# Kernel tuning notes

Measured on AMD Instinct MI355X. Metric: run time of the kernel, lower is better.

## Reference

```python
import jax, jax.numpy as jnp
import numpy as np

H = 64  # hidden size

def lstm_layer(x, h0, c0, Wih, Whh, bih, bhh):
    # x: [B,T,D]; Wih: [4H,D]; Whh: [4H,H]; gate order i,f,g,o (PyTorch)
    xp = jnp.einsum('btd,gd->btg', x, Wih) + bih  # precompute input projections [B,T,4H]
    def step(carry, xt):
        h, c = carry
        gates = xt + h @ Whh.T + bhh
        i, f, g, o = jnp.split(gates, 4, axis=-1)
        c = jax.nn.sigmoid(f) * c + jax.nn.sigmoid(i) * jnp.tanh(g)
        h = jax.nn.sigmoid(o) * jnp.tanh(c)
        return (h, c), h
    (_, _), ys = jax.lax.scan(step, (h0, c0), jnp.swapaxes(xp, 0, 1))  # scan over T
    return jnp.swapaxes(ys, 0, 1)  # [B,T,H]

def setup_inputs() -> dict:
    key = jax.random.key(0)
    ks = jax.random.split(key, 12)
    B, T = 256, 2048
    s = 0.1
    return {
        'input': jax.random.normal(ks[0], (B, T), jnp.float32),
        'h0': jnp.zeros((2, B, H), jnp.float32),
        'c0': jnp.zeros((2, B, H), jnp.float32),
        'Wih0': jax.random.normal(ks[1], (4 * H, 1), jnp.float32) * s,
        'Whh0': jax.random.normal(ks[2], (4 * H, H), jnp.float32) * s,
        'bih0': jax.random.normal(ks[3], (4 * H,), jnp.float32) * s,
        'bhh0': jax.random.normal(ks[4], (4 * H,), jnp.float32) * s,
        'Wih1': jax.random.normal(ks[5], (4 * H, H), jnp.float32) * s,
        'Whh1': jax.random.normal(ks[6], (4 * H, H), jnp.float32) * s,
        'bih1': jax.random.normal(ks[7], (4 * H,), jnp.float32) * s,
        'bhh1': jax.random.normal(ks[8], (4 * H,), jnp.float32) * s,
        'Wlin': jax.random.normal(ks[9], (1, H), jnp.float32) * s,
        'blin': jax.random.normal(ks[10], (1,), jnp.float32) * s,
    }

def reference(input, h0, c0, Wih0, Whh0, bih0, bhh0, Wih1, Whh1, bih1, bhh1, Wlin, blin):
    x = input[..., None]  # [B,T,1]
    y0 = lstm_layer(x, h0[0], c0[0], Wih0, Whh0, bih0, bhh0)
    y1 = lstm_layer(y0, h0[1], c0[1], Wih1, Whh1, bih1, bhh1)
    pred = jnp.einsum('bth,oh->bto', y1, Wlin) + blin  # [B,T,1]
    return pred[..., 0]
```

## Files before the change

### kernel.cpp

```cpp
#include <hip/hip_runtime.h>

#define HD 64
#define KP 16
#define NS 32
#define L2E 1.4426950408889634f

typedef _Float16 v2h __attribute__((ext_vector_type(2)));
typedef _Float16 h8  __attribute__((ext_vector_type(8)));

__device__ __forceinline__ float fexp2(float x) { return __builtin_amdgcn_exp2f(x); }
__device__ __forceinline__ float frcp(float x)  { return __builtin_amdgcn_rcpf(x); }
__device__ __forceinline__ float ftanh_fast(float x) {
    return 1.f - 2.f * frcp(fexp2(2.f * L2E * x) + 1.f);
}
__device__ __forceinline__ float fsig(float x) {
    return frcp(fexp2(-L2E * x) + 1.f);
}

#if __has_builtin(__builtin_amdgcn_fdot2)
__device__ __forceinline__ float FDOT2(v2h a, v2h b, float c) {
    return __builtin_amdgcn_fdot2(a, b, c, false);
}
#else
__device__ __forceinline__ float FDOT2(v2h a, v2h b, float c) {
    return fmaf((float)a.x, (float)b.x, fmaf((float)a.y, (float)b.y, c));
}
#endif


#define DECL32(P) \
    v2h P##_0,P##_1,P##_2,P##_3,P##_4,P##_5,P##_6,P##_7, \
        P##_8,P##_9,P##_10,P##_11,P##_12,P##_13,P##_14,P##_15, \
        P##_16,P##_17,P##_18,P##_19,P##_20,P##_21,P##_22,P##_23, \
        P##_24,P##_25,P##_26,P##_27,P##_28,P##_29,P##_30,P##_31

#define CVT2(v) v2h{(_Float16)v.x, (_Float16)v.y}
#define CVT2H(v) v2h{(_Float16)v.z, (_Float16)v.w}

#define LOAD32(W, r, P) do { \
    const float4* wp_ = (const float4*)((W) + (size_t)(r) * HD); \
    float4 v_; \
    v_=wp_[0];  P##_0 =CVT2(v_); P##_1 =CVT2H(v_); \
    v_=wp_[1];  P##_2 =CVT2(v_); P##_3 =CVT2H(v_); \
    v_=wp_[2];  P##_4 =CVT2(v_); P##_5 =CVT2H(v_); \
    v_=wp_[3];  P##_6 =CVT2(v_); P##_7 =CVT2H(v_); \
    v_=wp_[4];  P##_8 =CVT2(v_); P##_9 =CVT2H(v_); \
    v_=wp_[5];  P##_10=CVT2(v_); P##_11=CVT2H(v_); \
    v_=wp_[6];  P##_12=CVT2(v_); P##_13=CVT2H(v_); \
    v_=wp_[7];  P##_14=CVT2(v_); P##_15=CVT2H(v_); \
    v_=wp_[8];  P##_16=CVT2(v_); P##_17=CVT2H(v_); \
    v_=wp_[9];  P##_18=CVT2(v_); P##_19=CVT2H(v_); \
    v_=wp_[10]; P##_20=CVT2(v_); P##_21=CVT2H(v_); \
    v_=wp_[11]; P##_22=CVT2(v_); P##_23=CVT2H(v_); \
    v_=wp_[12]; P##_24=CVT2(v_); P##_25=CVT2H(v_); \
    v_=wp_[13]; P##_26=CVT2(v_); P##_27=CVT2H(v_); \
    v_=wp_[14]; P##_28=CVT2(v_); P##_29=CVT2H(v_); \
    v_=wp_[15]; P##_30=CVT2(v_); P##_31=CVT2H(v_); \
} while (0)

#define DOTG(P, i0, i1, i2, i3, A0, A1) \
    A0 = FDOT2(P##_##i0, p0_, A0); A1 = FDOT2(P##_##i1, p1_, A1); \
    A0 = FDOT2(P##_##i2, p2_, A0); A1 = FDOT2(P##_##i3, p3_, A1);

#define DOTBLK4(HP, q, i0, i1, i2, i3) \
    { h8 hv_ = (HP)[q]; \
      v2h p0_={hv_[0],hv_[1]}, p1_={hv_[2],hv_[3]}; \
      v2h p2_={hv_[4],hv_[5]}, p3_={hv_[6],hv_[7]}; \
      DOTG(wgA, i0,i1,i2,i3, a00,a01) DOTG(wgB, i0,i1,i2,i3, a10,a11) \
      DOTG(wgC, i0,i1,i2,i3, a20,a21) DOTG(wgD, i0,i1,i2,i3, a30,a31) }

#define DOT4N(HP) \
    DOTBLK4(HP,0, 0,1,2,3)     DOTBLK4(HP,1, 4,5,6,7) \
    DOTBLK4(HP,2, 8,9,10,11)   DOTBLK4(HP,3, 12,13,14,15) \
    DOTBLK4(HP,4, 16,17,18,19) DOTBLK4(HP,5, 20,21,22,23) \
    DOTBLK4(HP,6, 24,25,26,27) DOTBLK4(HP,7, 28,29,30,31)

#define DOTBLK2(HP, q, i0, i1, i2, i3) \
    { h8 hv_ = (HP)[q]; \
      v2h p0_={hv_[0],hv_[1]}, p1_={hv_[2],hv_[3]}; \
      v2h p2_={hv_[4],hv_[5]}, p3_={hv_[6],hv_[7]}; \
      DOTG(wgA, i0,i1,i2,i3, a00,a01) DOTG(wgB, i0,i1,i2,i3, a10,a11) }

#define DOT2N(HP) \
    DOTBLK2(HP,0, 0,1,2,3)     DOTBLK2(HP,1, 4,5,6,7) \
    DOTBLK2(HP,2, 8,9,10,11)   DOTBLK2(HP,3, 12,13,14,15) \
    DOTBLK2(HP,4, 16,17,18,19) DOTBLK2(HP,5, 20,21,22,23) \
    DOTBLK2(HP,6, 24,25,26,27) DOTBLK2(HP,7, 28,29,30,31)

__launch_bounds__(320, 1)
__global__ void lstm2_kernel(const float* __restrict__ x,
                             const float* __restrict__ h0in,
                             const float* __restrict__ c0in,
                             const float* __restrict__ Wih0,
                             const float* __restrict__ Whh0,
                             const float* __restrict__ bih0,
                             const float* __restrict__ bhh0,
                             const float* __restrict__ Wih1,
                             const float* __restrict__ Whh1,
                             const float* __restrict__ bih1,
                             const float* __restrict__ bhh1,
                             const float* __restrict__ Wlin,
                             const float* __restrict__ blin,
                             float* __restrict__ out,
                             int B, int T)
{
    const int b    = blockIdx.x;
    const int tid  = threadIdx.x;
    const int wave = tid >> 6;
    const int lane = tid & 63;

    __shared__ __align__(16) _Float16 h0ring[NS][HD];
    __shared__ __align__(16) _Float16 h1ring[NS][HD];
    __shared__ __align__(16) float    h1f32[NS][HD + 4];
    __shared__ __align__(16) float    xpring[NS][4][HD];

    {
        _Float16* z0 = &h0ring[0][0];
        for (int i = tid; i < NS * HD; i += 320) z0[i] = (_Float16)0.f;
        _Float16* z1 = &h1ring[0][0];
        for (int i = tid; i < NS * HD; i += 320) z1[i] = (_Float16)0.f;
        float* z2 = &h1f32[0][0];
        for (int i = tid; i < NS * (HD + 4); i += 320) z2[i] = 0.f;
        float* z3 = &xpring[0][0][0];
        for (int i = tid; i < NS * 4 * HD; i += 320) z3[i] = 0.f;
    }
    __syncthreads();

    const int nphase = (T + KP - 1) / KP + 3;

    if (wave == 0) {
        DECL32(wgA); DECL32(wgB); DECL32(wgC); DECL32(wgD);
        LOAD32(Whh0, lane,        wgA);
        LOAD32(Whh0, 64 + lane,   wgB);
        LOAD32(Whh0, 128 + lane,  wgC);
        LOAD32(Whh0, 192 + lane,  wgD);
        const float b0 = bih0[lane]       + bhh0[lane];
        const float b1 = bih0[64 + lane]  + bhh0[64 + lane];
        const float b2 = bih0[128 + lane] + bhh0[128 + lane];
        const float b3 = bih0[192 + lane] + bhh0[192 + lane];
        const float wx0 = Wih0[lane];       const float wx1 = Wih0[64 + lane];
        const float wx2 = Wih0[128 + lane]; const float wx3 = Wih0[192 + lane];
        float cst = c0in[b * HD + lane];
        h0ring[NS - 1][lane] = (_Float16)h0in[b * HD + lane];
        const float* xrow = x + (size_t)b * T;
        __syncthreads();

        for (int p = 0; p < nphase; ++p) {
            const int t0 = p * KP;
            if (t0 < T) {
                #pragma unroll 1
                for (int k = 0; k < KP; ++k) {
                    const int t = t0 + k;
                    if (t >= T) break;
                    const float xv = xrow[t];
                    const h8* hp = (const h8*)h0ring[(t + NS - 1) & (NS - 1)];
                    float a00 = b0, a01 = 0.f, a10 = b1, a11 = 0.f;
                    float a20 = b2, a21 = 0.f, a30 = b3, a31 = 0.f;
                    DOT4N(hp);
                    const float ai = fmaf(wx0, xv, a00 + a01);
                    const float af = fmaf(wx1, xv, a10 + a11);
                    const float ag = fmaf(wx2, xv, a20 + a21);
                    const float ao = fmaf(wx3, xv, a30 + a31);
                    const float iv = fsig(ai), fv = fsig(af);
                    const float gv = ftanh_fast(ag), ov = fsig(ao);
                    cst = fmaf(fv, cst, iv * gv);
                    const float h = ov * ftanh_fast(cst);
                    h0ring[t & (NS - 1)][lane] = (_Float16)h;
                }
            }
            __syncthreads();
        }
    } else if (wave == 1) {
        DECL32(wgA); DECL32(wgB); DECL32(wgC); DECL32(wgD);
        LOAD32(Whh1, lane,        wgA);
        LOAD32(Whh1, 64 + lane,   wgB);
        LOAD32(Whh1, 128 + lane,  wgC);
        LOAD32(Whh1, 192 + lane,  wgD);
        float cst = c0in[B * HD + b * HD + lane];
        h1ring[NS - 1][lane] = (_Float16)h0in[B * HD + b * HD + lane];
        __syncthreads();

        for (int p = 0; p < nphase; ++p) {
            const int t0 = (p - 2) * KP;
            if (p >= 2 && t0 < T) {
                #pragma unroll 1
                for (int k = 0; k < KP; ++k) {
                    const int t = t0 + k;
                    if (t >= T) break;
                    const int s = t & (NS - 1);
                    const float x0 = xpring[s][0][lane];
                    const float x1 = xpring[s][1][lane];
                    const float x2 = xpring[s][2][lane];
                    const float x3 = xpring[s][3][lane];
                    const h8* hp = (const h8*)h1ring[(t + NS - 1) & (NS - 1)];
                    float a00 = 0.f, a01 = 0.f, a10 = 0.f, a11 = 0.f;
                    float a20 = 0.f, a21 = 0.f, a30 = 0.f, a31 = 0.f;
                    DOT4N(hp);
                    const float ai = x0 + a00 + a01;
                    const float af = x1 + a10 + a11;
                    const float ag = x2 + a20 + a21;
                    const float ao = x3 + a30 + a31;
                    const float iv = fsig(ai), fv = fsig(af);
                    const float gv = ftanh_fast(ag), ov = fsig(ao);
                    cst = fmaf(fv, cst, iv * gv);
                    const float h = ov * ftanh_fast(cst);
                    h1ring[s][lane] = (_Float16)h;
                    h1f32[s][lane]  = h;
                }
            }
            __syncthreads();
        }
    } else if (wave <= 3) {
        DECL32(wgA); DECL32(wgB);
        const int g0 = (wave - 2) * 2;
        LOAD32(Wih1, g0 * HD + lane,       wgA);
        LOAD32(Wih1, (g0 + 1) * HD + lane, wgB);
        const float b0 = bih1[g0 * HD + lane]       + bhh1[g0 * HD + lane];
        const float b1 = bih1[(g0 + 1) * HD + lane] + bhh1[(g0 + 1) * HD + lane];
        __syncthreads();

        for (int p = 0; p < nphase; ++p) {
            const int t0 = (p - 1) * KP;
            if (p >= 1 && t0 < T) {
                #pragma unroll 1
                for (int k = 0; k < KP; ++k) {
                    const int t = t0 + k;
                    if (t >= T) break;
                    const int s = t & (NS - 1);
                    const h8* hp = (const h8*)h0ring[s];
                    float a00 = b0, a01 = 0.f, a10 = b1, a11 = 0.f;
                    DOT2N(hp);
                    xpring[s][g0][lane]     = a00 + a01;
                    xpring[s][g0 + 1][lane] = a10 + a11;
                }
            }
            __syncthreads();
        }
    } else {
        const float blin0 = blin[0];
        __syncthreads();

        for (int p = 0; p < nphase; ++p) {
            const int t0 = (p - 3) * KP;
            if (p >= 3 && t0 < T && lane < KP) {
                const int t = t0 + lane;
                if (t < T) {
                    const float4* hv4 = (const float4*)h1f32[t & (NS - 1)];
                    const float4* wp  = (const float4*)Wlin;
                    float acc = blin0;
                    #pragma unroll
                    for (int q = 0; q < 16; ++q) {
                        const float4 hv = hv4[q];
                        const float4 wv = wp[q];
                        acc = fmaf(wv.x, hv.x, acc);
                        acc = fmaf(wv.y, hv.y, acc);
                        acc = fmaf(wv.z, hv.z, acc);
                        acc = fmaf(wv.w, hv.w, acc);
                    }
                    out[(size_t)b * T + t] = acc;
                }
            }
            __syncthreads();
        }
    }
}

extern "C" void kernel_launch(void* const* d_in, const int* in_sizes, int n_in,
                              void* d_out, int out_size, void* d_ws, size_t ws_size,
                              hipStream_t stream)
{
    const float* x    = (const float*)d_in[0];
    const float* h0   = (const float*)d_in[1];
    const float* c0   = (const float*)d_in[2];
    const float* Wih0 = (const float*)d_in[3];
    const float* Whh0 = (const float*)d_in[4];
    const float* bih0 = (const float*)d_in[5];
    const float* bhh0 = (const float*)d_in[6];
    const float* Wih1 = (const float*)d_in[7];
    const float* Whh1 = (const float*)d_in[8];
    const float* bih1 = (const float*)d_in[9];
    const float* bhh1 = (const float*)d_in[10];
    const float* Wlin = (const float*)d_in[11];
    const float* blin = (const float*)d_in[12];
    float* out = (float*)d_out;

    const int B = in_sizes[1] / (2 * HD);
    const int T = in_sizes[0] / B;

    lstm2_kernel<<<dim3(B), dim3(320), 0, stream>>>(
        x, h0, c0, Wih0, Whh0, bih0, bhh0,
        Wih1, Whh1, bih1, bhh1, Wlin, blin, out, B, T);
}
```

Baseline: 986.8 us.

## Merge layer-1 input projection into one wave and pad LDS to force one block per CU

The two waves that each computed half of the layer-1 input projection are merged into a single wave holding all four gate weight rows, so the block shrinks from 320 to 256 threads (4 waves). A dummy 32KB shared buffer plus a waves_per_eu(1,1) attribute is added, apparently to limit residency to one block per CU and give each wave more registers. The merged wave does twice the dot-product work per timestep, which may lengthen that pipeline stage relative to the recurrent waves.

```diff
diff --git a/kernel.cpp b/kernel.cpp
--- a/kernel.cpp
+++ b/kernel.cpp
@@ -26,7 +26,6 @@
     return fmaf((float)a.x, (float)b.x, fmaf((float)a.y, (float)b.y, c));
 }
 #endif
-
 
 #define DECL32(P) \
     v2h P##_0,P##_1,P##_2,P##_3,P##_4,P##_5,P##_6,P##_7, \
@@ -75,34 +74,22 @@
     DOTBLK4(HP,4, 16,17,18,19) DOTBLK4(HP,5, 20,21,22,23) \
     DOTBLK4(HP,6, 24,25,26,27) DOTBLK4(HP,7, 28,29,30,31)
 
-#define DOTBLK2(HP, q, i0, i1, i2, i3) \
-    { h8 hv_ = (HP)[q]; \
-      v2h p0_={hv_[0],hv_[1]}, p1_={hv_[2],hv_[3]}; \
-      v2h p2_={hv_[4],hv_[5]}, p3_={hv_[6],hv_[7]}; \
-      DOTG(wgA, i0,i1,i2,i3, a00,a01) DOTG(wgB, i0,i1,i2,i3, a10,a11) }
-
-#define DOT2N(HP) \
-    DOTBLK2(HP,0, 0,1,2,3)     DOTBLK2(HP,1, 4,5,6,7) \
-    DOTBLK2(HP,2, 8,9,10,11)   DOTBLK2(HP,3, 12,13,14,15) \
-    DOTBLK2(HP,4, 16,17,18,19) DOTBLK2(HP,5, 20,21,22,23) \
-    DOTBLK2(HP,6, 24,25,26,27) DOTBLK2(HP,7, 28,29,30,31)
-
-__launch_bounds__(320, 1)
-__global__ void lstm2_kernel(const float* __restrict__ x,
-                             const float* __restrict__ h0in,
-                             const float* __restrict__ c0in,
-                             const float* __restrict__ Wih0,
-                             const float* __restrict__ Whh0,
-                             const float* __restrict__ bih0,
-                             const float* __restrict__ bhh0,
-                             const float* __restrict__ Wih1,
-                             const float* __restrict__ Whh1,
-                             const float* __restrict__ bih1,
-                             const float* __restrict__ bhh1,
-                             const float* __restrict__ Wlin,
-                             const float* __restrict__ blin,
-                             float* __restrict__ out,
-                             int B, int T)
+__global__ __launch_bounds__(256) __attribute__((amdgpu_waves_per_eu(1, 1)))
+void lstm2_kernel(const float* __restrict__ x,
+                  const float* __restrict__ h0in,
+                  const float* __restrict__ c0in,
+                  const float* __restrict__ Wih0,
+                  const float* __restrict__ Whh0,
+                  const float* __restrict__ bih0,
+                  const float* __restrict__ bhh0,
+                  const float* __restrict__ Wih1,
+                  const float* __restrict__ Whh1,
+                  const float* __restrict__ bih1,
+                  const float* __restrict__ bhh1,
+                  const float* __restrict__ Wlin,
+                  const float* __restrict__ blin,
+                  float* __restrict__ out,
+                  int B, int T)
 {
     const int b    = blockIdx.x;
     const int tid  = threadIdx.x;
@@ -113,18 +100,21 @@
     __shared__ __align__(16) _Float16 h1ring[NS][HD];
     __shared__ __align__(16) float    h1f32[NS][HD + 4];
     __shared__ __align__(16) float    xpring[NS][4][HD];
+    __shared__ float ldspad[8192];
 
     {
         _Float16* z0 = &h0ring[0][0];
-        for (int i = tid; i < NS * HD; i += 320) z0[i] = (_Float16)0.f;
+        for (int i = tid; i < NS * HD; i += 256) z0[i] = (_Float16)0.f;
         _Float16* z1 = &h1ring[0][0];
-        for (int i = tid; i < NS * HD; i += 320) z1[i] = (_Float16)0.f;
+        for (int i = tid; i < NS * HD; i += 256) z1[i] = (_Float16)0.f;
         float* z2 = &h1f32[0][0];
-        for (int i = tid; i < NS * (HD + 4); i += 320) z2[i] = 0.f;
+        for (int i = tid; i < NS * (HD + 4); i += 256) z2[i] = 0.f;
         float* z3 = &xpring[0][0][0];
-        for (int i = tid; i < NS * 4 * HD; i += 320) z3[i] = 0.f;
+        for (int i = tid; i < NS * 4 * HD; i += 256) z3[i] = 0.f;
+        ldspad[tid] = 0.f;
     }
     __syncthreads();
+    { float pv = ldspad[tid]; asm volatile("" :: "v"(pv)); }
 
     const int nphase = (T + KP - 1) / KP + 3;
 
@@ -210,13 +200,16 @@
             }
             __syncthreads();
         }
-    } else if (wave <= 3) {
-        DECL32(wgA); DECL32(wgB);
-        const int g0 = (wave - 2) * 2;
-        LOAD32(Wih1, g0 * HD + lane,       wgA);
-        LOAD32(Wih1, (g0 + 1) * HD + lane, wgB);
-        const float b0 = bih1[g0 * HD + lane]       + bhh1[g0 * HD + lane];
-        const float b1 = bih1[(g0 + 1) * HD + lane] + bhh1[(g0 + 1) * HD + lane];
+    } else if (wave == 2) {
+        DECL32(wgA); DECL32(wgB); DECL32(wgC); DECL32(wgD);
+        LOAD32(Wih1, lane,        wgA);
+        LOAD32(Wih1, 64 + lane,   wgB);
+        LOAD32(Wih1, 128 + lane,  wgC);
+        LOAD32(Wih1, 192 + lane,  wgD);
+        const float b0 = bih1[lane]       + bhh1[lane];
+        const float b1 = bih1[64 + lane]  + bhh1[64 + lane];
+        const float b2 = bih1[128 + lane] + bhh1[128 + lane];
+        const float b3 = bih1[192 + lane] + bhh1[192 + lane];
         __syncthreads();
 
         for (int p = 0; p < nphase; ++p) {
@@ -229,9 +222,12 @@
                     const int s = t & (NS - 1);
                     const h8* hp = (const h8*)h0ring[s];
                     float a00 = b0, a01 = 0.f, a10 = b1, a11 = 0.f;
-                    DOT2N(hp);
-                    xpring[s][g0][lane]     = a00 + a01;
-                    xpring[s][g0 + 1][lane] = a10 + a11;
+                    float a20 = b2, a21 = 0.f, a30 = b3, a31 = 0.f;
+                    DOT4N(hp);
+                    xpring[s][0][lane] = a00 + a01;
+                    xpring[s][1][lane] = a10 + a11;
+                    xpring[s][2][lane] = a20 + a21;
+                    xpring[s][3][lane] = a30 + a31;
                 }
             }
             __syncthreads();
@@ -287,7 +283,7 @@
     const int B = in_sizes[1] / (2 * HD);
     const int T = in_sizes[0] / B;
 
-    lstm2_kernel<<<dim3(B), dim3(320), 0, stream>>>(
+    lstm2_kernel<<<dim3(B), dim3(256), 0, stream>>>(
         x, h0, c0, Wih0, Whh0, bih0, bhh0,
         Wih1, Whh1, bih1, bhh1, Wlin, blin, out, B, T);
 }
```

Measured after the change: 991.3 us. Within noise of the previous version (+0.5%).

## Split recurrent weights between registers and LDS, shrink block to four waves

Applied to the files above, without the earlier changes.

The recurrent waves now hold only the first half of each Whh row in registers as packed fp16. The second half is staged once into padded fp16 LDS tables and read during each step's dot product. The separate output-projection wave is merged into the second input-projection wave, so the block drops from five waves to four and launch bounds no longer force one block per CU. The aim is lower register pressure and higher occupancy. In exchange, every recurrent step does extra LDS reads on the serial critical path, and the merged wave carries more work per phase.

```diff
diff --git a/kernel.cpp b/kernel.cpp
--- a/kernel.cpp
+++ b/kernel.cpp
@@ -27,6 +27,13 @@
 }
 #endif
 
+
+#define CVT2(v)  v2h{(_Float16)v.x, (_Float16)v.y}
+#define CVT2H(v) v2h{(_Float16)v.z, (_Float16)v.w}
+
+#define DECL16(P) \
+    v2h P##_0,P##_1,P##_2,P##_3,P##_4,P##_5,P##_6,P##_7, \
+        P##_8,P##_9,P##_10,P##_11,P##_12,P##_13,P##_14,P##_15
 
 #define DECL32(P) \
     v2h P##_0,P##_1,P##_2,P##_3,P##_4,P##_5,P##_6,P##_7, \
@@ -34,8 +41,18 @@
         P##_16,P##_17,P##_18,P##_19,P##_20,P##_21,P##_22,P##_23, \
         P##_24,P##_25,P##_26,P##_27,P##_28,P##_29,P##_30,P##_31
 
-#define CVT2(v) v2h{(_Float16)v.x, (_Float16)v.y}
-#define CVT2H(v) v2h{(_Float16)v.z, (_Float16)v.w}
+#define LOAD16(W, r, P) do { \
+    const float4* wp_ = (const float4*)((W) + (size_t)(r) * HD); \
+    float4 v_; \
+    v_=wp_[0];  P##_0 =CVT2(v_); P##_1 =CVT2H(v_); \
+    v_=wp_[1];  P##_2 =CVT2(v_); P##_3 =CVT2H(v_); \
+    v_=wp_[2];  P##_4 =CVT2(v_); P##_5 =CVT2H(v_); \
+    v_=wp_[3];  P##_6 =CVT2(v_); P##_7 =CVT2H(v_); \
+    v_=wp_[4];  P##_8 =CVT2(v_); P##_9 =CVT2H(v_); \
+    v_=wp_[5];  P##_10=CVT2(v_); P##_11=CVT2H(v_); \
+    v_=wp_[6];  P##_12=CVT2(v_); P##_13=CVT2H(v_); \
+    v_=wp_[7];  P##_14=CVT2(v_); P##_15=CVT2H(v_); \
+} while (0)
 
 #define LOAD32(W, r, P) do { \
     const float4* wp_ = (const float4*)((W) + (size_t)(r) * HD); \
@@ -62,18 +79,35 @@
     A0 = FDOT2(P##_##i0, p0_, A0); A1 = FDOT2(P##_##i1, p1_, A1); \
     A0 = FDOT2(P##_##i2, p2_, A0); A1 = FDOT2(P##_##i3, p3_, A1);
 
-#define DOTBLK4(HP, q, i0, i1, i2, i3) \
+#define DOTBLK4R(HP, q, i0, i1, i2, i3) \
     { h8 hv_ = (HP)[q]; \
       v2h p0_={hv_[0],hv_[1]}, p1_={hv_[2],hv_[3]}; \
       v2h p2_={hv_[4],hv_[5]}, p3_={hv_[6],hv_[7]}; \
       DOTG(wgA, i0,i1,i2,i3, a00,a01) DOTG(wgB, i0,i1,i2,i3, a10,a11) \
       DOTG(wgC, i0,i1,i2,i3, a20,a21) DOTG(wgD, i0,i1,i2,i3, a30,a31) }
 
-#define DOT4N(HP) \
-    DOTBLK4(HP,0, 0,1,2,3)     DOTBLK4(HP,1, 4,5,6,7) \
-    DOTBLK4(HP,2, 8,9,10,11)   DOTBLK4(HP,3, 12,13,14,15) \
-    DOTBLK4(HP,4, 16,17,18,19) DOTBLK4(HP,5, 20,21,22,23) \
-    DOTBLK4(HP,6, 24,25,26,27) DOTBLK4(HP,7, 28,29,30,31)
+#define DOTBLK4L(HP, WL, jj, q) \
+    { h8 hv_ = (HP)[q]; \
+      v2h p0_={hv_[0],hv_[1]}, p1_={hv_[2],hv_[3]}; \
+      v2h p2_={hv_[4],hv_[5]}, p3_={hv_[6],hv_[7]}; \
+      h8 wa_ = *(const h8*)&(WL)[(jj)][8*((q)-4)]; \
+      h8 wb_ = *(const h8*)&(WL)[64+(jj)][8*((q)-4)]; \
+      h8 wc_ = *(const h8*)&(WL)[128+(jj)][8*((q)-4)]; \
+      h8 wd_ = *(const h8*)&(WL)[192+(jj)][8*((q)-4)]; \
+      a00=FDOT2(v2h{wa_[0],wa_[1]},p0_,a00); a01=FDOT2(v2h{wa_[2],wa_[3]},p1_,a01); \
+      a00=FDOT2(v2h{wa_[4],wa_[5]},p2_,a00); a01=FDOT2(v2h{wa_[6],wa_[7]},p3_,a01); \
+      a10=FDOT2(v2h{wb_[0],wb_[1]},p0_,a10); a11=FDOT2(v2h{wb_[2],wb_[3]},p1_,a11); \
+      a10=FDOT2(v2h{wb_[4],wb_[5]},p2_,a10); a11=FDOT2(v2h{wb_[6],wb_[7]},p3_,a11); \
+      a20=FDOT2(v2h{wc_[0],wc_[1]},p0_,a20); a21=FDOT2(v2h{wc_[2],wc_[3]},p1_,a21); \
+      a20=FDOT2(v2h{wc_[4],wc_[5]},p2_,a20); a21=FDOT2(v2h{wc_[6],wc_[7]},p3_,a21); \
+      a30=FDOT2(v2h{wd_[0],wd_[1]},p0_,a30); a31=FDOT2(v2h{wd_[2],wd_[3]},p1_,a31); \
+      a30=FDOT2(v2h{wd_[4],wd_[5]},p2_,a30); a31=FDOT2(v2h{wd_[6],wd_[7]},p3_,a31); }
+
+#define DOT4H(HP, WL, jj) \
+    DOTBLK4R(HP,0, 0,1,2,3)    DOTBLK4R(HP,1, 4,5,6,7) \
+    DOTBLK4R(HP,2, 8,9,10,11)  DOTBLK4R(HP,3, 12,13,14,15) \
+    DOTBLK4L(HP,WL,jj,4) DOTBLK4L(HP,WL,jj,5) \
+    DOTBLK4L(HP,WL,jj,6) DOTBLK4L(HP,WL,jj,7)
 
 #define DOTBLK2(HP, q, i0, i1, i2, i3) \
     { h8 hv_ = (HP)[q]; \
@@ -87,28 +121,30 @@
     DOTBLK2(HP,4, 16,17,18,19) DOTBLK2(HP,5, 20,21,22,23) \
     DOTBLK2(HP,6, 24,25,26,27) DOTBLK2(HP,7, 28,29,30,31)
 
-__launch_bounds__(320, 1)
-__global__ void lstm2_kernel(const float* __restrict__ x,
-                             const float* __restrict__ h0in,
-                             const float* __restrict__ c0in,
-                             const float* __restrict__ Wih0,
-                             const float* __restrict__ Whh0,
-                             const float* __restrict__ bih0,
-                             const float* __restrict__ bhh0,
-                             const float* __restrict__ Wih1,
-                             const float* __restrict__ Whh1,
-                             const float* __restrict__ bih1,
-                             const float* __restrict__ bhh1,
-                             const float* __restrict__ Wlin,
-                             const float* __restrict__ blin,
-                             float* __restrict__ out,
-                             int B, int T)
+__global__ __launch_bounds__(256)
+void lstm2_kernel(const float* __restrict__ x,
+                  const float* __restrict__ h0in,
+                  const float* __restrict__ c0in,
+                  const float* __restrict__ Wih0,
+                  const float* __restrict__ Whh0,
+                  const float* __restrict__ bih0,
+                  const float* __restrict__ bhh0,
+                  const float* __restrict__ Wih1,
+                  const float* __restrict__ Whh1,
+                  const float* __restrict__ bih1,
+                  const float* __restrict__ bhh1,
+                  const float* __restrict__ Wlin,
+                  const float* __restrict__ blin,
+                  float* __restrict__ out,
+                  int B, int T)
 {
     const int b    = blockIdx.x;
     const int tid  = threadIdx.x;
-    const int wave = tid >> 6;
+    const int wave = __builtin_amdgcn_readfirstlane(tid >> 6);
     const int lane = tid & 63;
 
+    __shared__ __align__(16) _Float16 wlA[256][72];
+    __shared__ __align__(16) _Float16 wlC[256][72];
     __shared__ __align__(16) _Float16 h0ring[NS][HD];
     __shared__ __align__(16) _Float16 h1ring[NS][HD];
     __shared__ __align__(16) float    h1f32[NS][HD + 4];
@@ -116,24 +152,40 @@
 
     {
         _Float16* z0 = &h0ring[0][0];
-        for (int i = tid; i < NS * HD; i += 320) z0[i] = (_Float16)0.f;
+        for (int i = tid; i < NS * HD; i += 256) z0[i] = (_Float16)0.f;
         _Float16* z1 = &h1ring[0][0];
-        for (int i = tid; i < NS * HD; i += 320) z1[i] = (_Float16)0.f;
+        for (int i = tid; i < NS * HD; i += 256) z1[i] = (_Float16)0.f;
         float* z2 = &h1f32[0][0];
-        for (int i = tid; i < NS * (HD + 4); i += 320) z2[i] = 0.f;
+        for (int i = tid; i < NS * (HD + 4); i += 256) z2[i] = 0.f;
         float* z3 = &xpring[0][0][0];
-        for (int i = tid; i < NS * 4 * HD; i += 320) z3[i] = 0.f;
+        for (int i = tid; i < NS * 4 * HD; i += 256) z3[i] = 0.f;
+    }
+    {
+        const int r = tid;
+        const float4* a4 = (const float4*)(Whh0 + (size_t)r * HD + 32);
+        const float4* c4 = (const float4*)(Whh1 + (size_t)r * HD + 32);
+        #pragma unroll
+        for (int q0 = 0; q0 < 4; ++q0) {
+            float4 u = a4[2 * q0], v = a4[2 * q0 + 1];
+            *(h8*)&wlA[r][8 * q0] =
+                h8{(_Float16)u.x, (_Float16)u.y, (_Float16)u.z, (_Float16)u.w,
+                   (_Float16)v.x, (_Float16)v.y, (_Float16)v.z, (_Float16)v.w};
+            float4 u2 = c4[2 * q0], v2 = c4[2 * q0 + 1];
+            *(h8*)&wlC[r][8 * q0] =
+                h8{(_Float16)u2.x, (_Float16)u2.y, (_Float16)u2.z, (_Float16)u2.w,
+                   (_Float16)v2.x, (_Float16)v2.y, (_Float16)v2.z, (_Float16)v2.w};
+        }
     }
     __syncthreads();
 
     const int nphase = (T + KP - 1) / KP + 3;
 
     if (wave == 0) {
-        DECL32(wgA); DECL32(wgB); DECL32(wgC); DECL32(wgD);
-        LOAD32(Whh0, lane,        wgA);
-        LOAD32(Whh0, 64 + lane,   wgB);
-        LOAD32(Whh0, 128 + lane,  wgC);
-        LOAD32(Whh0, 192 + lane,  wgD);
+        DECL16(wgA); DECL16(wgB); DECL16(wgC); DECL16(wgD);
+        LOAD16(Whh0, lane,        wgA);
+        LOAD16(Whh0, 64 + lane,   wgB);
+        LOAD16(Whh0, 128 + lane,  wgC);
+        LOAD16(Whh0, 192 + lane,  wgD);
         const float b0 = bih0[lane]       + bhh0[lane];
         const float b1 = bih0[64 + lane]  + bhh0[64 + lane];
         const float b2 = bih0[128 + lane] + bhh0[128 + lane];
@@ -156,7 +208,7 @@
                     const h8* hp = (const h8*)h0ring[(t + NS - 1) & (NS - 1)];
                     float a00 = b0, a01 = 0.f, a10 = b1, a11 = 0.f;
                     float a20 = b2, a21 = 0.f, a30 = b3, a31 = 0.f;
-                    DOT4N(hp);
+                    DOT4H(hp, wlA, lane);
                     const float ai = fmaf(wx0, xv, a00 + a01);
                     const float af = fmaf(wx1, xv, a10 + a11);
                     const float ag = fmaf(wx2, xv, a20 + a21);
@@ -171,11 +223,11 @@
             __syncthreads();
         }
     } else if (wave == 1) {
-        DECL32(wgA); DECL32(wgB); DECL32(wgC); DECL32(wgD);
-        LOAD32(Whh1, lane,        wgA);
-        LOAD32(Whh1, 64 + lane,   wgB);
-        LOAD32(Whh1, 128 + lane,  wgC);
-        LOAD32(Whh1, 192 + lane,  wgD);
+        DECL16(wgA); DECL16(wgB); DECL16(wgC); DECL16(wgD);
+        LOAD16(Whh1, lane,        wgA);
+        LOAD16(Whh1, 64 + lane,   wgB);
+        LOAD16(Whh1, 128 + lane,  wgC);
+        LOAD16(Whh1, 192 + lane,  wgD);
         float cst = c0in[B * HD + b * HD + lane];
         h1ring[NS - 1][lane] = (_Float16)h0in[B * HD + b * HD + lane];
         __syncthreads();
@@ -195,7 +247,7 @@
                     const h8* hp = (const h8*)h1ring[(t + NS - 1) & (NS - 1)];
                     float a00 = 0.f, a01 = 0.f, a10 = 0.f, a11 = 0.f;
                     float a20 = 0.f, a21 = 0.f, a30 = 0.f, a31 = 0.f;
-                    DOT4N(hp);
+                    DOT4H(hp, wlC, lane);
                     const float ai = x0 + a00 + a01;
                     const float af = x1 + a10 + a11;
                     const float ag = x2 + a20 + a21;
@@ -210,13 +262,12 @@
             }
             __syncthreads();
         }
-    } else if (wave <= 3) {
+    } else if (wave == 2) {
         DECL32(wgA); DECL32(wgB);
-        const int g0 = (wave - 2) * 2;
-        LOAD32(Wih1, g0 * HD + lane,       wgA);
-        LOAD32(Wih1, (g0 + 1) * HD + lane, wgB);
-        const float b0 = bih1[g0 * HD + lane]       + bhh1[g0 * HD + lane];
-        const float b1 = bih1[(g0 + 1) * HD + lane] + bhh1[(g0 + 1) * HD + lane];
+        LOAD32(Wih1, lane,      wgA);
+        LOAD32(Wih1, 64 + lane, wgB);
+        const float b0 = bih1[lane]      + bhh1[lane];
+        const float b1 = bih1[64 + lane] + bhh1[64 + lane];
         __syncthreads();
 
         for (int p = 0; p < nphase; ++p) {
@@ -230,20 +281,39 @@
                     const h8* hp = (const h8*)h0ring[s];
                     float a00 = b0, a01 = 0.f, a10 = b1, a11 = 0.f;
                     DOT2N(hp);
-                    xpring[s][g0][lane]     = a00 + a01;
-                    xpring[s][g0 + 1][lane] = a10 + a11;
+                    xpring[s][0][lane] = a00 + a01;
+                    xpring[s][1][lane] = a10 + a11;
                 }
             }
             __syncthreads();
         }
     } else {
+        DECL32(wgA); DECL32(wgB);
+        LOAD32(Wih1, 128 + lane, wgA);
+        LOAD32(Wih1, 192 + lane, wgB);
+        const float b2 = bih1[128 + lane] + bhh1[128 + lane];
+        const float b3 = bih1[192 + lane] + bhh1[192 + lane];
         const float blin0 = blin[0];
         __syncthreads();
 
         for (int p = 0; p < nphase; ++p) {
-            const int t0 = (p - 3) * KP;
-            if (p >= 3 && t0 < T && lane < KP) {
-                const int t = t0 + lane;
+            const int t0 = (p - 1) * KP;
+            if (p >= 1 && t0 < T) {
+                #pragma unroll 1
+                for (int k = 0; k < KP; ++k) {
+                    const int t = t0 + k;
+                    if (t >= T) break;
+                    const int s = t & (NS - 1);
+                    const h8* hp = (const h8*)h0ring[s];
+                    float a00 = b2, a01 = 0.f, a10 = b3, a11 = 0.f;
+                    DOT2N(hp);
+                    xpring[s][2][lane] = a00 + a01;
+                    xpring[s][3][lane] = a10 + a11;
+                }
+            }
+            const int t0h = (p - 3) * KP;
+            if (p >= 3 && t0h < T && lane < KP) {
+                const int t = t0h + lane;
                 if (t < T) {
                     const float4* hv4 = (const float4*)h1f32[t & (NS - 1)];
                     const float4* wp  = (const float4*)Wlin;
@@ -287,7 +357,7 @@
     const int B = in_sizes[1] / (2 * HD);
     const int T = in_sizes[0] / B;
 
-    lstm2_kernel<<<dim3(B), dim3(320), 0, stream>>>(
+    lstm2_kernel<<<dim3(B), dim3(256), 0, stream>>>(
         x, h0, c0, Wih0, Whh0, bih0, bhh0,
         Wih1, Whh1, bih1, bhh1, Wlin, blin, out, B, T);
 }
```

Result: slower. 1.234 ms (+25.1%).
